# Performance work log

Hardware: AMD Instinct MI355X
Metric: run time of the kernel (lower is better)

The kernel has to match this reference:

```python
import jax, jax.numpy as jnp
import numpy as np

N_LAYER, N_HEAD, N_EMBD, BLOCK, B, T = 8, 8, 1024, 1024, 2, 1024
LN_EPS = 1e-5


def _ln(x, w, b):
    m = jnp.mean(x, axis=-1, keepdims=True)
    v = jnp.mean(jnp.square(x - m), axis=-1, keepdims=True)
    return (x - m) * jax.lax.rsqrt(v + LN_EPS) * w + b


def setup_inputs() -> dict:
    key = jax.random.key(0)
    ks = jax.random.split(key, 8)
    L, C = N_LAYER, N_EMBD
    rn = lambda k, shape, s=0.02: jax.random.normal(k, shape, jnp.float32) * s
    return {
        "x": jax.random.normal(ks[0], (B, T, C), jnp.float32),
        "wpe": rn(ks[1], (BLOCK, C)),
        "ln1_w": jnp.ones((L, C), jnp.float32),
        "ln1_b": jnp.zeros((L, C), jnp.float32),
        "attn_w": rn(ks[2], (L, 3 * C, C)),
        "attn_b": jnp.zeros((L, 3 * C), jnp.float32),
        "proj_w": rn(ks[3], (L, C, C), 0.02 / np.sqrt(2 * L)),
        "proj_b": jnp.zeros((L, C), jnp.float32),
        "ln2_w": jnp.ones((L, C), jnp.float32),
        "ln2_b": jnp.zeros((L, C), jnp.float32),
        "fc_w": rn(ks[4], (L, 4 * C, C)),
        "fc_b": jnp.zeros((L, 4 * C), jnp.float32),
        "fcp_w": rn(ks[5], (L, C, 4 * C), 0.02 / np.sqrt(2 * L)),
        "fcp_b": jnp.zeros((L, C), jnp.float32),
        "lnf_w": jnp.ones((C,), jnp.float32),
        "lnf_b": jnp.zeros((C,), jnp.float32),
    }


def reference(x, wpe, ln1_w, ln1_b, attn_w, attn_b, proj_w, proj_b,
              ln2_w, ln2_b, fc_w, fc_b, fcp_w, fcp_b, lnf_w, lnf_b):
    Bb, Tt, C = x.shape
    H = N_HEAD
    D = C // H
    scale = jnp.float32(1.0 / np.sqrt(D))
    h = x + wpe[:Tt][None]  # pos emb broadcast over batch; dropout = identity (eval)
    causal = jnp.tril(jnp.ones((Tt, Tt), bool))  # [T,T]

    def block(h, p):
        l1w, l1b, aw, ab, pw, pb, l2w, l2b, fw, fb, pw2, pb2 = p
        xn = _ln(h, l1w, l1b)
        qkv = xn @ aw.T + ab  # [B,T,3C]
        q, k, v = jnp.split(qkv, 3, axis=-1)
        q = q.reshape(Bb, Tt, H, D).transpose(0, 2, 1, 3)  # bhtd
        k = k.reshape(Bb, Tt, H, D).transpose(0, 2, 1, 3)
        v = v.reshape(Bb, Tt, H, D).transpose(0, 2, 1, 3)
        att = jnp.einsum('bhtd,bhsd->bhts', q, k) * scale
        att = jnp.where(causal, att, -jnp.inf)
        att = jax.nn.softmax(att, axis=-1)
        y = jnp.einsum('bhts,bhsd->bhtd', att, v)
        y = y.transpose(0, 2, 1, 3).reshape(Bb, Tt, C)
        h = h + (y @ pw.T + pb)
        xn2 = _ln(h, l2w, l2b)
        m = jax.nn.gelu(xn2 @ fw.T + fb, approximate=True)  # matches NewGELU tanh form
        h = h + (m @ pw2.T + pb2)
        return h, None

    h, _ = jax.lax.scan(block, h, (ln1_w, ln1_b, attn_w, attn_b, proj_w, proj_b,
                                   ln2_w, ln2_b, fc_w, fc_b, fcp_w, fcp_b))
    return _ln(h, lnf_w, lnf_b)
```

## Files before the change

### kernel.cpp

```cpp
#include <hip/hip_runtime.h>

typedef unsigned short u16;
typedef __attribute__((ext_vector_type(8))) short short8;
typedef __attribute__((ext_vector_type(4))) float floatx4;

__device__ __forceinline__ u16 f2b(float f){
  unsigned u = __builtin_bit_cast(unsigned, f);
  u += 0x7FFFu + ((u >> 16) & 1u);
  return (u16)(u >> 16);
}

__device__ __forceinline__ float gelu_f(float x){
  float u = 0.7978845608028654f * (x + 0.044715f * x * x * x);
  float e = __expf(2.0f * u);
  return 0.5f * x * (2.0f - 2.0f / (e + 1.0f));
}

typedef const __attribute__((address_space(1))) unsigned int gas_u32;
typedef __attribute__((address_space(3))) unsigned int las_u32;
__device__ __forceinline__ void gll16(const void* g, void* l){
  __builtin_amdgcn_global_load_lds((gas_u32*)g, (las_u32*)l, 16, 0, 0);
}

__global__ __launch_bounds__(256) void k_cvt(const float* __restrict__ src,
                                             u16* __restrict__ dst){
  size_t e = ((size_t)blockIdx.x * 256 + threadIdx.x) * 4;
  float4 v = *(const float4*)(src + e);
  ushort4 o; o.x = f2b(v.x); o.y = f2b(v.y); o.z = f2b(v.z); o.w = f2b(v.w);
  *(ushort4*)(dst + e) = o;
}

__global__ __launch_bounds__(256) void k_addpos(const float* __restrict__ x,
                                                const float* __restrict__ wpe,
                                                float* __restrict__ h){
  size_t e = ((size_t)blockIdx.x * 256 + threadIdx.x) * 4;
  float4 a = *(const float4*)(x + e);
  float4 p = *(const float4*)(wpe + (e & 1048575u));
  float4 o; o.x = a.x + p.x; o.y = a.y + p.y; o.z = a.z + p.z; o.w = a.w + p.w;
  *(float4*)(h + e) = o;
}

__global__ __launch_bounds__(256) void k_layernorm(const float* __restrict__ x,
                                                   const float* __restrict__ w,
                                                   const float* __restrict__ b,
                                                   void* __restrict__ out, int out_bf16){
  int row = blockIdx.x, t = threadIdx.x;
  const float* xr = x + (size_t)row * 1024;
  float4 v = ((const float4*)xr)[t];
  float s1 = v.x + v.y + v.z + v.w;
  float s2 = v.x*v.x + v.y*v.y + v.z*v.z + v.w*v.w;
  #pragma unroll
  for (int off = 32; off > 0; off >>= 1){
    s1 += __shfl_down(s1, off);
    s2 += __shfl_down(s2, off);
  }
  __shared__ float p1[4], p2[4];
  if ((t & 63) == 0){ p1[t >> 6] = s1; p2[t >> 6] = s2; }
  __syncthreads();
  float S1 = p1[0] + p1[1] + p1[2] + p1[3];
  float S2 = p2[0] + p2[1] + p2[2] + p2[3];
  float mean = S1 * (1.0f / 1024.0f);
  float var  = S2 * (1.0f / 1024.0f) - mean * mean;
  float rs = rsqrtf(var + 1e-5f);
  float4 wv = ((const float4*)w)[t];
  float4 bv = ((const float4*)b)[t];
  float o0 = (v.x - mean) * rs * wv.x + bv.x;
  float o1 = (v.y - mean) * rs * wv.y + bv.y;
  float o2 = (v.z - mean) * rs * wv.z + bv.z;
  float o3 = (v.w - mean) * rs * wv.w + bv.w;
  if (out_bf16){
    ushort4 o; o.x = f2b(o0); o.y = f2b(o1); o.z = f2b(o2); o.w = f2b(o3);
    ((ushort4*)((u16*)out + (size_t)row * 1024))[t] = o;
  } else {
    float4 o; o.x = o0; o.y = o1; o.z = o2; o.w = o3;
    ((float4*)((float*)out + (size_t)row * 1024))[t] = o;
  }
}

template<int MODE>
__global__ __launch_bounds__(256) void k_gemm(
    const u16* __restrict__ A, int lda,
    const u16* __restrict__ B, int ldb,
    const float* __restrict__ bias,
    void* __restrict__ Out, int ldo,
    int Kdim, int n_ntiles, int Ksplit,
    u16* __restrict__ Out2)
{
  int bx = blockIdx.x, by = blockIdx.y;
  int nt = bx % n_ntiles, sp = bx / n_ntiles;
  int m0 = by * 128, n0 = nt * 128;
  int ks = sp * Ksplit;
  int ke = ks + Ksplit < Kdim ? ks + Ksplit : Kdim;
  if (ks >= ke) return;

  __shared__ u16 As[2][128 * 32];
  __shared__ u16 Bs[2][128 * 32];
  int t = threadIdx.x;
  int lane = t & 63, wid = t >> 6;
  int wm = (wid >> 1) * 64, wn = (wid & 1) * 64;
  int quad = lane >> 4, tm = lane & 15;
  int ar = t >> 2, ac = (t & 3) * 8;
  const u16* Ab = A + (size_t)(m0 + ar) * lda + ac;
  const u16* Bb = B + (size_t)(n0 + ar) * ldb + ac;
  const size_t a64 = (size_t)64 * lda, b64 = (size_t)64 * ldb;

  floatx4 acc[4][4] = {};
  gll16(Ab + ks,       &As[0][t * 8]);
  gll16(Ab + a64 + ks, &As[0][2048 + t * 8]);
  gll16(Bb + ks,       &Bs[0][t * 8]);
  gll16(Bb + b64 + ks, &Bs[0][2048 + t * 8]);
  __syncthreads();

  int cur = 0;
  for (int k0 = ks; k0 < ke; k0 += 32){
    int k1 = k0 + 32;
    if (k1 < ke){
      gll16(Ab + k1,       &As[cur ^ 1][t * 8]);
      gll16(Ab + a64 + k1, &As[cur ^ 1][2048 + t * 8]);
      gll16(Bb + k1,       &Bs[cur ^ 1][t * 8]);
      gll16(Bb + b64 + k1, &Bs[cur ^ 1][2048 + t * 8]);
    }
    short8 af[4], bf[4];
    #pragma unroll
    for (int i = 0; i < 4; i++)
      af[i] = *(const short8*)&As[cur][(wm + i * 16 + tm) * 32 + quad * 8];
    #pragma unroll
    for (int j = 0; j < 4; j++)
      bf[j] = *(const short8*)&Bs[cur][(wn + j * 16 + tm) * 32 + quad * 8];
    #pragma unroll
    for (int i = 0; i < 4; i++)
      #pragma unroll
      for (int j = 0; j < 4; j++)
        acc[i][j] = __builtin_amdgcn_mfma_f32_16x16x32_bf16(af[i], bf[j], acc[i][j], 0, 0, 0);
    __syncthreads();
    cur ^= 1;
  }

  if (MODE == 3 && n0 >= 2048){
    #pragma unroll
    for (int j = 0; j < 4; j++){
      int col = n0 + wn + j * 16 + tm;
      float bc = bias ? bias[col] : 0.0f;
      int dg = col - 2048;
      int hh = dg >> 7, d = dg & 127;
      #pragma unroll
      for (int i = 0; i < 4; i++){
        int row0 = m0 + wm + i * 16 + quad * 4;
        int b = row0 >> 10, s = row0 & 1023;
        ushort4 o;
        o.x = f2b(acc[i][j][0] + bc);
        o.y = f2b(acc[i][j][1] + bc);
        o.z = f2b(acc[i][j][2] + bc);
        o.w = f2b(acc[i][j][3] + bc);
        *(ushort4*)(Out2 + (size_t)(b * 8 + hh) * 131072 + (size_t)d * 1024 + s) = o;
      }
    }
  } else {
    #pragma unroll
    for (int j = 0; j < 4; j++){
      int col = n0 + wn + j * 16 + tm;
      float bc = 0.0f;
      if ((MODE == 0 || MODE == 1 || MODE == 3) && bias) bc = bias[col];
      if (MODE == 2 && sp == 0 && bias) bc = bias[col];
      #pragma unroll
      for (int i = 0; i < 4; i++){
        int row0 = m0 + wm + i * 16 + quad * 4;
        #pragma unroll
        for (int r = 0; r < 4; r++){
          float v = acc[i][j][r] + bc;
          size_t idx = (size_t)(row0 + r) * ldo + col;
          if (MODE == 0 || MODE == 3) ((u16*)Out)[idx] = f2b(v);
          else if (MODE == 1)         ((u16*)Out)[idx] = f2b(gelu_f(v));
          else                        atomicAdd((float*)Out + idx, v);
        }
      }
    }
  }
}

__global__ __launch_bounds__(256) void k_flash(const u16* __restrict__ qkv,
                                               const u16* __restrict__ vt,
                                               u16* __restrict__ yb){
  int qi = blockIdx.x, bh = blockIdx.y;
  int b = bh >> 3, hh = bh & 7;
  int t = threadIdx.x, lane = t & 63, w = t >> 6;
  int quad = lane >> 4, tm = lane & 15;
  const int q0 = qi * 64;
  const u16* Qg  = qkv + (size_t)b * 3145728 + hh * 128;
  const u16* Kg  = Qg + 1024;
  const u16* Vtg = vt + (size_t)bh * 131072;
  __shared__ u16 Ks[2][64 * 128];
  __shared__ u16 Vs[2][128 * 64];
  __shared__ u16 Ps[4][16 * 64];

  auto stage = [&](int s0s, int bufi){
    int idx = w * 256 + lane;
    #pragma unroll
    for (int p = 0; p < 4; p++){
      int id = idx + p * 64;
      gll16(Kg + (size_t)(s0s + (id >> 4)) * 3072 + (id & 15) * 8, &Ks[bufi][id * 8]);
    }
    #pragma unroll
    for (int p = 0; p < 4; p++){
      int id = idx + p * 64;
      gll16(Vtg + (size_t)(id >> 3) * 1024 + s0s + (id & 7) * 8, &Vs[bufi][id * 8]);
    }
  };

  short8 qf[4];
  {
    const u16* qr = Qg + (size_t)(q0 + w * 16 + tm) * 3072 + quad * 8;
    #pragma unroll
    for (int kk = 0; kk < 4; kk++) qf[kk] = *(const short8*)(qr + kk * 32);
  }
  floatx4 o_acc[8] = {};
  float m_r[4], l_r[4];
  #pragma unroll
  for (int r = 0; r < 4; r++){ m_r[r] = -3.0e38f; l_r[r] = 0.0f; }
  const float scale = 0.08838834764831845f;

  stage(0, 0);
  __syncthreads();
  int cur = 0;
  for (int s0 = 0; s0 <= q0; s0 += 64){
    if (s0 + 64 <= q0) stage(s0 + 64, cur ^ 1);
    floatx4 s_acc[4] = {};
    #pragma unroll
    for (int j = 0; j < 4; j++)
      #pragma unroll
      for (int kk = 0; kk < 4; kk++){
        short8 kf = *(const short8*)&Ks[cur][(j * 16 + tm) * 128 + kk * 32 + quad * 8];
        s_acc[j] = __builtin_amdgcn_mfma_f32_16x16x32_bf16(qf[kk], kf, s_acc[j], 0, 0, 0);
      }
    bool diag = (s0 == q0);
    float sv[4][4];
    #pragma unroll
    for (int j = 0; j < 4; j++)
      #pragma unroll
      for (int r = 0; r < 4; r++){
        float v = s_acc[j][r] * scale;
        if (diag && (j * 16 + tm > w * 16 + quad * 4 + r)) v = -3.0e38f;
        sv[j][r] = v;
      }
    float pv[4][4];
    #pragma unroll
    for (int r = 0; r < 4; r++){
      float m = fmaxf(fmaxf(sv[0][r], sv[1][r]), fmaxf(sv[2][r], sv[3][r]));
      #pragma unroll
      for (int off = 8; off > 0; off >>= 1) m = fmaxf(m, __shfl_xor(m, off));
      float m_new = fmaxf(m_r[r], m);
      float alpha = __expf(m_r[r] - m_new);
      m_r[r] = m_new;
      float s = 0.0f;
      #pragma unroll
      for (int j = 0; j < 4; j++){
        float p = __expf(sv[j][r] - m_new);
        pv[j][r] = p; s += p;
      }
      #pragma unroll
      for (int off = 8; off > 0; off >>= 1) s += __shfl_xor(s, off);
      l_r[r] = l_r[r] * alpha + s;
      #pragma unroll
      for (int jd = 0; jd < 8; jd++) o_acc[jd][r] *= alpha;
    }
    u16* Pw = Ps[w];
    #pragma unroll
    for (int j = 0; j < 4; j++)
      #pragma unroll
      for (int r = 0; r < 4; r++)
        Pw[(quad * 4 + r) * 64 + j * 16 + tm] = f2b(pv[j][r]);
    asm volatile("s_waitcnt lgkmcnt(0)" ::: "memory");
    short8 pf[2];
    #pragma unroll
    for (int kk = 0; kk < 2; kk++)
      pf[kk] = *(const short8*)&Pw[tm * 64 + kk * 32 + quad * 8];
    #pragma unroll
    for (int jd = 0; jd < 8; jd++)
      #pragma unroll
      for (int kk = 0; kk < 2; kk++){
        short8 vf = *(const short8*)&Vs[cur][(jd * 16 + tm) * 64 + kk * 32 + quad * 8];
        o_acc[jd] = __builtin_amdgcn_mfma_f32_16x16x32_bf16(pf[kk], vf, o_acc[jd], 0, 0, 0);
      }
    __syncthreads();
    cur ^= 1;
  }
  u16* yr = yb + ((size_t)b * 1024 + q0 + w * 16 + quad * 4) * 1024 + hh * 128;
  #pragma unroll
  for (int r = 0; r < 4; r++){
    float inv = 1.0f / l_r[r];
    #pragma unroll
    for (int jd = 0; jd < 8; jd++)
      yr[(size_t)r * 1024 + jd * 16 + tm] = f2b(o_acc[jd][r] * inv);
  }
}

extern "C" void kernel_launch(void* const* d_in, const int* in_sizes, int n_in,
                              void* d_out, int out_size, void* d_ws, size_t ws_size,
                              hipStream_t stream){
  const float* x     = (const float*)d_in[0];
  const float* wpe   = (const float*)d_in[1];
  const float* ln1w  = (const float*)d_in[2];
  const float* ln1b  = (const float*)d_in[3];
  const float* attnw = (const float*)d_in[4];
  const float* attnb = (const float*)d_in[5];
  const float* projw = (const float*)d_in[6];
  const float* projb = (const float*)d_in[7];
  const float* ln2w  = (const float*)d_in[8];
  const float* ln2b  = (const float*)d_in[9];
  const float* fcw   = (const float*)d_in[10];
  const float* fcb   = (const float*)d_in[11];
  const float* fcpw  = (const float*)d_in[12];
  const float* fcpb  = (const float*)d_in[13];
  const float* lnfw  = (const float*)d_in[14];
  const float* lnfb  = (const float*)d_in[15];

  char* ws = (char*)d_ws;
  float* h    = (float*)(ws);
  u16*   xn   = (u16*)(ws + 8388608);
  u16*   qkv  = (u16*)(ws + 12582912);
  u16*   vt   = (u16*)(ws + 25165824);
  u16*   yb   = (u16*)(ws + 29360128);
  u16*   mlp  = (u16*)(ws + 33554432);
  u16*   wqkv = (u16*)(ws + 50331648);
  u16*   wprj = (u16*)(ws + 100663296);
  u16*   wfc  = (u16*)(ws + 117440512);
  u16*   wfcp = (u16*)(ws + 184549376);

  k_cvt<<<24576, 256, 0, stream>>>(attnw, wqkv);
  k_cvt<<<8192,  256, 0, stream>>>(projw, wprj);
  k_cvt<<<32768, 256, 0, stream>>>(fcw,  wfc);
  k_cvt<<<32768, 256, 0, stream>>>(fcpw, wfcp);
  k_addpos<<<2048, 256, 0, stream>>>(x, wpe, h);

  for (int l = 0; l < 8; l++){
    k_layernorm<<<2048, 256, 0, stream>>>(h, ln1w + l * 1024, ln1b + l * 1024, xn, 1);
    k_gemm<3><<<dim3(24, 16), 256, 0, stream>>>(
        xn, 1024, wqkv + (size_t)l * 3145728, 1024, attnb + l * 3072,
        qkv, 3072, 1024, 24, 1024, vt);
    k_flash<<<dim3(16, 16), 256, 0, stream>>>(qkv, vt, yb);
    k_gemm<2><<<dim3(32, 16), 256, 0, stream>>>(
        yb, 1024, wprj + (size_t)l * 1048576, 1024, projb + l * 1024,
        h, 1024, 1024, 8, 256, (u16*)nullptr);
    k_layernorm<<<2048, 256, 0, stream>>>(h, ln2w + l * 1024, ln2b + l * 1024, xn, 1);
    k_gemm<1><<<dim3(32, 16), 256, 0, stream>>>(
        xn, 1024, wfc + (size_t)l * 4194304, 1024, fcb + l * 4096,
        mlp, 4096, 1024, 32, 1024, (u16*)nullptr);
    k_gemm<2><<<dim3(32, 16), 256, 0, stream>>>(
        mlp, 4096, wfcp + (size_t)l * 4194304, 4096, fcpb + l * 1024,
        h, 1024, 4096, 8, 1024, (u16*)nullptr);
  }
  k_layernorm<<<2048, 256, 0, stream>>>(h, lnfw, lnfb, (float*)d_out, 0);
  (void)in_sizes; (void)n_in; (void)out_size; (void)ws_size;
}
```

Before: 2.058 ms.

## Swizzle LDS layouts, deepen GEMM K-tile, fuse weight conversions, add MFMA priority

The GEMM K-tile grows from 32 to 64 and its LDS tiles use an XOR swizzle so the MFMA fragment reads avoid bank conflicts. The flash-attention K, V and P shared buffers get the same swizzle, and the MFMA phases are wrapped in s_setprio. The four weight-conversion launches are merged into one kernel that picks its source and destination by block index. LDS per GEMM block doubles, which can reduce occupancy.

```diff
diff --git a/kernel.cpp b/kernel.cpp
--- a/kernel.cpp
+++ b/kernel.cpp
@@ -22,12 +22,21 @@
   __builtin_amdgcn_global_load_lds((gas_u32*)g, (las_u32*)l, 16, 0, 0);
 }
 
-__global__ __launch_bounds__(256) void k_cvt(const float* __restrict__ src,
-                                             u16* __restrict__ dst){
-  size_t e = ((size_t)blockIdx.x * 256 + threadIdx.x) * 4;
-  float4 v = *(const float4*)(src + e);
+__global__ __launch_bounds__(256) void k_cvt4(
+    const float* __restrict__ s0, u16* __restrict__ d0,
+    const float* __restrict__ s1, u16* __restrict__ d1,
+    const float* __restrict__ s2, u16* __restrict__ d2,
+    const float* __restrict__ s3, u16* __restrict__ d3){
+  int blk = blockIdx.x;
+  const float* s; u16* d; size_t bb;
+  if      (blk < 24576){ s = s0; d = d0; bb = blk; }
+  else if (blk < 32768){ s = s1; d = d1; bb = blk - 24576; }
+  else if (blk < 65536){ s = s2; d = d2; bb = blk - 32768; }
+  else                 { s = s3; d = d3; bb = blk - 65536; }
+  size_t e = (bb * 256 + threadIdx.x) * 4;
+  float4 v = *(const float4*)(s + e);
   ushort4 o; o.x = f2b(v.x); o.y = f2b(v.y); o.z = f2b(v.z); o.w = f2b(v.w);
-  *(ushort4*)(dst + e) = o;
+  *(ushort4*)(d + e) = o;
 }
 
 __global__ __launch_bounds__(256) void k_addpos(const float* __restrict__ x,
@@ -93,45 +102,52 @@
   int ke = ks + Ksplit < Kdim ? ks + Ksplit : Kdim;
   if (ks >= ke) return;
 
-  __shared__ u16 As[2][128 * 32];
-  __shared__ u16 Bs[2][128 * 32];
+  __shared__ u16 As[2][128 * 64];
+  __shared__ u16 Bs[2][128 * 64];
   int t = threadIdx.x;
   int lane = t & 63, wid = t >> 6;
   int wm = (wid >> 1) * 64, wn = (wid & 1) * 64;
   int quad = lane >> 4, tm = lane & 15;
-  int ar = t >> 2, ac = (t & 3) * 8;
-  const u16* Ab = A + (size_t)(m0 + ar) * lda + ac;
-  const u16* Bb = B + (size_t)(n0 + ar) * ldb + ac;
-  const size_t a64 = (size_t)64 * lda, b64 = (size_t)64 * ldb;
+  int r0 = t >> 3, sl = t & 7;
+  int scol = (sl ^ (r0 & 7)) * 8;
+  const u16* Asrc = A + (size_t)(m0 + r0) * lda + scol;
+  const u16* Bsrc = B + (size_t)(n0 + r0) * ldb + scol;
+  const size_t a32 = (size_t)32 * lda, b32 = (size_t)32 * ldb;
 
   floatx4 acc[4][4] = {};
-  gll16(Ab + ks,       &As[0][t * 8]);
-  gll16(Ab + a64 + ks, &As[0][2048 + t * 8]);
-  gll16(Bb + ks,       &Bs[0][t * 8]);
-  gll16(Bb + b64 + ks, &Bs[0][2048 + t * 8]);
+  #pragma unroll
+  for (int c = 0; c < 4; c++){
+    gll16(Asrc + c * a32 + ks, &As[0][c * 2048 + t * 8]);
+    gll16(Bsrc + c * b32 + ks, &Bs[0][c * 2048 + t * 8]);
+  }
   __syncthreads();
 
   int cur = 0;
-  for (int k0 = ks; k0 < ke; k0 += 32){
-    int k1 = k0 + 32;
+  for (int k0 = ks; k0 < ke; k0 += 64){
+    int k1 = k0 + 64;
     if (k1 < ke){
-      gll16(Ab + k1,       &As[cur ^ 1][t * 8]);
-      gll16(Ab + a64 + k1, &As[cur ^ 1][2048 + t * 8]);
-      gll16(Bb + k1,       &Bs[cur ^ 1][t * 8]);
-      gll16(Bb + b64 + k1, &Bs[cur ^ 1][2048 + t * 8]);
-    }
-    short8 af[4], bf[4];
-    #pragma unroll
-    for (int i = 0; i < 4; i++)
-      af[i] = *(const short8*)&As[cur][(wm + i * 16 + tm) * 32 + quad * 8];
-    #pragma unroll
-    for (int j = 0; j < 4; j++)
-      bf[j] = *(const short8*)&Bs[cur][(wn + j * 16 + tm) * 32 + quad * 8];
-    #pragma unroll
-    for (int i = 0; i < 4; i++)
+      #pragma unroll
+      for (int c = 0; c < 4; c++){
+        gll16(Asrc + c * a32 + k1, &As[cur ^ 1][c * 2048 + t * 8]);
+        gll16(Bsrc + c * b32 + k1, &Bs[cur ^ 1][c * 2048 + t * 8]);
+      }
+    }
+    #pragma unroll
+    for (int kk = 0; kk < 2; kk++){
+      short8 af[4], bf[4];
+      int cx = (kk * 32 + quad * 8) ^ ((tm & 7) << 3);
+      #pragma unroll
+      for (int i = 0; i < 4; i++)
+        af[i] = *(const short8*)&As[cur][(wm + i * 16 + tm) * 64 + cx];
       #pragma unroll
       for (int j = 0; j < 4; j++)
-        acc[i][j] = __builtin_amdgcn_mfma_f32_16x16x32_bf16(af[i], bf[j], acc[i][j], 0, 0, 0);
+        bf[j] = *(const short8*)&Bs[cur][(wn + j * 16 + tm) * 64 + cx];
+      #pragma unroll
+      for (int i = 0; i < 4; i++)
+        #pragma unroll
+        for (int j = 0; j < 4; j++)
+          acc[i][j] = __builtin_amdgcn_mfma_f32_16x16x32_bf16(af[i], bf[j], acc[i][j], 0, 0, 0);
+    }
     __syncthreads();
     cur ^= 1;
   }
@@ -198,12 +214,14 @@
     #pragma unroll
     for (int p = 0; p < 4; p++){
       int id = idx + p * 64;
-      gll16(Kg + (size_t)(s0s + (id >> 4)) * 3072 + (id & 15) * 8, &Ks[bufi][id * 8]);
+      int s = id >> 4, slk = id & 15;
+      gll16(Kg + (size_t)(s0s + s) * 3072 + ((slk ^ (s & 7)) * 8), &Ks[bufi][id * 8]);
     }
     #pragma unroll
     for (int p = 0; p < 4; p++){
       int id = idx + p * 64;
-      gll16(Vtg + (size_t)(id >> 3) * 1024 + s0s + (id & 7) * 8, &Vs[bufi][id * 8]);
+      int d = id >> 3, slv = id & 7;
+      gll16(Vtg + (size_t)d * 1024 + s0s + ((slv ^ (d & 7)) * 8), &Vs[bufi][id * 8]);
     }
   };
 
@@ -225,13 +243,16 @@
   for (int s0 = 0; s0 <= q0; s0 += 64){
     if (s0 + 64 <= q0) stage(s0 + 64, cur ^ 1);
     floatx4 s_acc[4] = {};
+    __builtin_amdgcn_s_setprio(1);
     #pragma unroll
     for (int j = 0; j < 4; j++)
       #pragma unroll
       for (int kk = 0; kk < 4; kk++){
-        short8 kf = *(const short8*)&Ks[cur][(j * 16 + tm) * 128 + kk * 32 + quad * 8];
+        short8 kf = *(const short8*)&Ks[cur][(j * 16 + tm) * 128 +
+                        ((kk * 32 + quad * 8) ^ ((tm & 7) << 3))];
         s_acc[j] = __builtin_amdgcn_mfma_f32_16x16x32_bf16(qf[kk], kf, s_acc[j], 0, 0, 0);
       }
+    __builtin_amdgcn_s_setprio(0);
     bool diag = (s0 == q0);
     float sv[4][4];
     #pragma unroll
@@ -267,20 +288,25 @@
     #pragma unroll
     for (int j = 0; j < 4; j++)
       #pragma unroll
-      for (int r = 0; r < 4; r++)
-        Pw[(quad * 4 + r) * 64 + j * 16 + tm] = f2b(pv[j][r]);
+      for (int r = 0; r < 4; r++){
+        int pr = quad * 4 + r;
+        Pw[pr * 64 + ((j * 16 + tm) ^ ((pr & 7) << 3))] = f2b(pv[j][r]);
+      }
     asm volatile("s_waitcnt lgkmcnt(0)" ::: "memory");
     short8 pf[2];
     #pragma unroll
     for (int kk = 0; kk < 2; kk++)
-      pf[kk] = *(const short8*)&Pw[tm * 64 + kk * 32 + quad * 8];
+      pf[kk] = *(const short8*)&Pw[tm * 64 + ((kk * 32 + quad * 8) ^ ((tm & 7) << 3))];
+    __builtin_amdgcn_s_setprio(1);
     #pragma unroll
     for (int jd = 0; jd < 8; jd++)
       #pragma unroll
       for (int kk = 0; kk < 2; kk++){
-        short8 vf = *(const short8*)&Vs[cur][(jd * 16 + tm) * 64 + kk * 32 + quad * 8];
+        short8 vf = *(const short8*)&Vs[cur][(jd * 16 + tm) * 64 +
+                        ((kk * 32 + quad * 8) ^ ((tm & 7) << 3))];
         o_acc[jd] = __builtin_amdgcn_mfma_f32_16x16x32_bf16(pf[kk], vf, o_acc[jd], 0, 0, 0);
       }
+    __builtin_amdgcn_s_setprio(0);
     __syncthreads();
     cur ^= 1;
   }
@@ -326,10 +352,7 @@
   u16*   wfc  = (u16*)(ws + 117440512);
   u16*   wfcp = (u16*)(ws + 184549376);
 
-  k_cvt<<<24576, 256, 0, stream>>>(attnw, wqkv);
-  k_cvt<<<8192,  256, 0, stream>>>(projw, wprj);
-  k_cvt<<<32768, 256, 0, stream>>>(fcw,  wfc);
-  k_cvt<<<32768, 256, 0, stream>>>(fcpw, wfcp);
+  k_cvt4<<<98304, 256, 0, stream>>>(attnw, wqkv, projw, wprj, fcw, wfc, fcpw, wfcp);
   k_addpos<<<2048, 256, 0, stream>>>(x, wpe, h);
 
   for (int l = 0; l < 8; l++){
```

New measurement: 1.859 ms. 1.11x faster.
